# Kernel optimization log

Hardware: AMD Instinct MI355X
Metric: run time of the kernel (lower is better)

The kernel has to match this reference:

```python
import jax, jax.numpy as jnp
import numpy as np

GAMMA = 1.05  # VoxelSampler.GAMMA


def setup_inputs() -> dict:
    key = jax.random.key(0)
    k1, k2, k3, k4, k5 = jax.random.split(key, 5)
    B, T, R, Np, F = 2, 8, 128, 32768, 5
    # point xy within pc_range, remaining features (z, intensity, ...) gaussian
    xy = jax.random.uniform(k1, (B, T, Np, 2), minval=-75.0, maxval=75.0)
    rest = jax.random.normal(k2, (B, T, Np, F - 2))
    points = jnp.concatenate([xy, rest], axis=-1)  # [B,T,Np,5]
    # rois: [cx,cy,cz, dx,dy,dz, yaw, vx,vy]
    ctr = jax.random.uniform(k3, (B, T, R, 3), minval=-75.0, maxval=75.0)
    dims = jax.random.uniform(k4, (B, T, R, 3), minval=1.0, maxval=6.0)
    yaw_vel = jax.random.normal(k5, (B, T, R, 3))
    trajectory_rois = jnp.concatenate([ctr, dims, yaw_vel], axis=-1)  # [B,T,R,9]
    return {"points": points, "trajectory_rois": trajectory_rois, "num_sample": 32}


def reference(points, trajectory_rois, num_sample):
    # points: [B,T,Np,5] (pre-partitioned per batch/frame, mirrors the
    # batch-column + timestamp masking of the torch code with static shapes)
    # trajectory_rois: [B,T,R,9]
    B, T, R, _ = trajectory_rois.shape
    Fdim = points.shape[-1]
    # speed = ||roi[..., -2:]||, per-roi gamma = clamp((1.05*(1+speed))**(t/5), max=2.5)
    speed = jnp.linalg.norm(trajectory_rois[..., 7:9], axis=-1)          # [B,T,R]
    t_idx = jnp.arange(T, dtype=points.dtype)
    gamma = jnp.minimum((GAMMA * (1.0 + speed)) ** (t_idx[None, :, None] / 5.0), 2.5)
    # cylindrical radius per roi: ||dims_xy/2|| * gamma
    radiis = jnp.linalg.norm(trajectory_rois[..., 3:5] * 0.5, axis=-1) * gamma  # [B,T,R]
    cx = trajectory_rois[..., 0]
    cy = trajectory_rois[..., 1]
    px = points[..., 0]
    py = points[..., 1]
    dx = px[:, :, None, :] - cx[..., None]   # [B,T,R,Np]
    dy = py[:, :, None, :] - cy[..., None]
    dis = jnp.sqrt(dx * dx + dy * dy)        # [B,T,R,Np]
    in_radius = (dis <= radiis[..., None]).astype(points.dtype)
    # topk over 0/1 mask: picks num_sample in-radius points (lowest indices first),
    # exactly like torch.topk(point_mask.float(), num_sample)
    vals, idx = jax.lax.top_k(in_radius, num_sample)  # [B,T,R,S]
    sampled = jnp.take_along_axis(points[:, :, None, :, :], idx[..., None], axis=3)  # [B,T,R,S,5]
    sampled = jnp.where(vals[..., None] > 0, sampled, jnp.zeros((), dtype=points.dtype))
    # stack frames -> permute(0,2,1,3,4) -> flatten(2,3): [B,R,T*S,5]
    out = jnp.transpose(sampled, (0, 2, 1, 3, 4)).reshape(B, R, T * num_sample, Fdim)
    return out
```

## Files before the change

kernel.cpp:

```cpp
#include <hip/hip_runtime.h>
#include <math.h>

#define B_   2
#define T_   8
#define R_   128
#define NP_  32768
#define F_   5
#define S_   32
#define NBT  (B_ * T_)
#define NROW (NBT * R_)
#define WV_  8
#define SEGPTS (NP_ / WV_)
#define NIT  (SEGPTS / 512)

__device__ __forceinline__ int mbcnt64(unsigned long long m) {
    return __builtin_amdgcn_mbcnt_hi((unsigned)(m >> 32),
           __builtin_amdgcn_mbcnt_lo((unsigned)m, 0u));
}

__global__ __launch_bounds__(256) void xy_transpose_prep(
    const float* __restrict__ points,
    const float* __restrict__ rois,
    float2* __restrict__ xy,
    float4* __restrict__ rowc)
{
    const int j = blockIdx.x * blockDim.x + threadIdx.x;
    if (j < NBT * NP_ / 4) {
        const float4* src = (const float4*)points + (size_t)j * 5;
        const float4 a = src[0], b = src[1], c = src[2], d = src[3], e = src[4];
        float4* dst = (float4*)xy + (size_t)j * 2;
        dst[0] = make_float4(a.x, a.y, b.y, b.z);
        dst[1] = make_float4(c.z, c.w, d.w, e.x);
    }
    if (j < NROW) {
        const int row = j;
        const int bt  = row / R_;
        const int t   = bt % T_;
        const float* roi = rois + (size_t)row * 9;
        const float cx = roi[0], cy = roi[1];
        const float hx = roi[3] * 0.5f, hy = roi[4] * 0.5f;
        const float vx = roi[7], vy = roi[8];
        const float speed  = sqrtf(vx * vx + vy * vy);
        const float base_g = 1.05f * (1.0f + speed);
        const float expo   = (float)t / 5.0f;
        const float gamma  = fminf((float)pow((double)base_g, (double)expo), 2.5f);
        const float radius = sqrtf(hx * hx + hy * hy) * gamma;
        unsigned ut = __float_as_uint(radius * radius);
        while (sqrtf(__uint_as_float(ut)) > radius) --ut;
        while (sqrtf(__uint_as_float(ut + 1u)) <= radius) ++ut;
        rowc[row] = make_float4(cx, cy, __uint_as_float(ut), 0.0f);
    }
}


#define PROC(qq, kk)                                                              \
    {                                                                             \
        const int idx0 = segbase + (it * 256 + (kk) * 64 + lane) * 2;             \
        {     \
            const float ax = __fsub_rn(qq.x, rc0.x), ay = __fsub_rn(qq.y, rc0.y); \
            const float bx = __fsub_rn(qq.z, rc0.x), by = __fsub_rn(qq.w, rc0.y); \
            const float d2a = __fadd_rn(__fmul_rn(ax, ax), __fmul_rn(ay, ay));    \
            const float d2b = __fadd_rn(__fmul_rn(bx, bx), __fmul_rn(by, by));    \
            const bool p0 = (d2a <= rc0.z), p1 = (d2b <= rc0.z);                  \
            const unsigned long long m0 = __ballot(p0), m1 = __ballot(p1);        \
            if (m0 | m1) {                                                        \
                const int base = sel0 + mbcnt64(m0) + mbcnt64(m1);                \
                if (p0 && base < S_) hitbuf[w][0][base] = (unsigned short)idx0;   \
                if (p1) { const int s2 = base + (p0 ? 1 : 0);                     \
                          if (s2 < S_) hitbuf[w][0][s2] = (unsigned short)(idx0 + 1); } \
                sel0 += __popcll(m0) + __popcll(m1);                              \
            }                                                                     \
        }                                                                         \
        {                             \
            const float ax = __fsub_rn(qq.x, rc1.x), ay = __fsub_rn(qq.y, rc1.y); \
            const float bx = __fsub_rn(qq.z, rc1.x), by = __fsub_rn(qq.w, rc1.y); \
            const float d2a = __fadd_rn(__fmul_rn(ax, ax), __fmul_rn(ay, ay));    \
            const float d2b = __fadd_rn(__fmul_rn(bx, bx), __fmul_rn(by, by));    \
            const bool p0 = (d2a <= rc1.z), p1 = (d2b <= rc1.z);                  \
            const unsigned long long m0 = __ballot(p0), m1 = __ballot(p1);        \
            if (m0 | m1) {                                                        \
                const int base = sel1 + mbcnt64(m0) + mbcnt64(m1);                \
                if (p0 && base < S_) hitbuf[w][1][base] = (unsigned short)idx0;   \
                if (p1) { const int s2 = base + (p0 ? 1 : 0);                     \
                          if (s2 < S_) hitbuf[w][1][s2] = (unsigned short)(idx0 + 1); } \
                sel1 += __popcll(m0) + __popcll(m1);                              \
            }                                                                     \
        }                                                                         \
    }

__global__ __launch_bounds__(512) void fused_scan_emit(
    const float2* __restrict__ xy,
    const float4* __restrict__ rowc,
    const float* __restrict__ points,
    float* __restrict__ out)
{
    __shared__ unsigned short hitbuf[WV_][2][S_];
    __shared__ int cnt[WV_][2];
    const int w    = threadIdx.x >> 6;
    const int lane = threadIdx.x & 63;
    const int row0 = blockIdx.x * 2;
    const int row1 = row0 + 1;
    const int bt   = row0 / R_;
    const float4 rc0 = rowc[row0], rc1 = rowc[row1];
    const int segbase = w * SEGPTS;

    const float4* src = (const float4*)(xy + (size_t)bt * NP_) + (segbase >> 1) + lane;
    int sel0 = 0, sel1 = 0;
    float4 q0 = src[0], q1 = src[64], q2 = src[128], q3 = src[192];
    src += 256;
    int it = 0;
    for (; it < NIT - 1; ++it) {
        const float4 t0 = src[0], t1 = src[64], t2 = src[128], t3 = src[192];
        src += 256;
        PROC(q0, 0) PROC(q1, 1) PROC(q2, 2) PROC(q3, 3)
        q0 = t0; q1 = t1; q2 = t2; q3 = t3;
        if (sel0 >= S_ && sel1 >= S_) break;
    }
    if (it == NIT - 1) { PROC(q0, 0) PROC(q1, 1) PROC(q2, 2) PROC(q3, 3) }

    if (lane == 0) {
        cnt[w][0] = (sel0 < S_) ? sel0 : S_;
        cnt[w][1] = (sel1 < S_) ? sel1 : S_;
    }
    __syncthreads();

    if (threadIdx.x < 64) {
        const int half = lane >> 5;
        const int s    = lane & 31;
        int seg = -1, local = 0, acc = 0;
        #pragma unroll
        for (int g = 0; g < WV_; ++g) {
            const int na = acc + cnt[g][half];
            if (seg < 0 && s < na) { seg = g; local = s - acc; }
            acc = na;
        }
        const int row = half ? row1 : row0;
        const int r = row % R_;
        const int t = bt % T_;
        const int b = bt / T_;
        float* o = out + ((((size_t)b * R_ + r) * T_ + t) * S_ + s) * (size_t)F_;
        if (seg >= 0) {
            const int pi = hitbuf[seg][half][local];
            const float* p = points + ((size_t)bt * NP_ + pi) * F_;
            o[0] = p[0]; o[1] = p[1]; o[2] = p[2]; o[3] = p[3]; o[4] = p[4];
        } else {
            o[0] = 0.0f; o[1] = 0.0f; o[2] = 0.0f; o[3] = 0.0f; o[4] = 0.0f;
        }
    }
}

extern "C" void kernel_launch(void* const* d_in, const int* in_sizes, int n_in,
                              void* d_out, int out_size, void* d_ws, size_t ws_size,
                              hipStream_t stream) {
    const float* points = (const float*)d_in[0];
    const float* rois   = (const float*)d_in[1];
    float* out = (float*)d_out;

    char* ws = (char*)d_ws;
    float2* xy   = (float2*)ws;
    float4* rowc = (float4*)(ws + 4194304);

    xy_transpose_prep<<<(NBT * NP_ / 4 + 255) / 256, 256, 0, stream>>>(points, rois, xy, rowc);

    fused_scan_emit<<<NROW / 2, 512, 0, stream>>>(xy, rowc, points, out);
}
```

Before: 82.53 us.

## Process four ROI rows per block sharing each loaded point tile

Each block now tests four ROI rows against every loaded chunk of point xy data instead of two, halving the number of blocks and the global/L2 reads of the xy buffer per row. The main loop is restructured as a manually double-buffered pair of loads with no unrolling, and the early-exit check once all rows have 32 hits is removed, so every wave always scans its full segment. Launch bounds request higher occupancy. The trade-off is more registers and ballots per iteration, and losing the early termination when rows fill quickly.

New measurement: 84.81 us. +2.8%, slower.

```diff
diff --git a/kernel.cpp b/kernel.cpp
--- a/kernel.cpp
+++ b/kernel.cpp
@@ -10,6 +10,8 @@
 #define NBT  (B_ * T_)
 #define NROW (NBT * R_)
 #define WV_  8
+#define RPB  4
+#define NBLK (NROW / RPB)
 #define SEGPTS (NP_ / WV_)
 #define NIT  (SEGPTS / 512)
 
@@ -53,94 +55,99 @@
 }
 
 
-#define PROC(qq, kk)                                                              \
+#define PROC1(qq, base, rc, sel, hb)                                              \
     {                                                                             \
-        const int idx0 = segbase + (it * 256 + (kk) * 64 + lane) * 2;             \
-        {     \
-            const float ax = __fsub_rn(qq.x, rc0.x), ay = __fsub_rn(qq.y, rc0.y); \
-            const float bx = __fsub_rn(qq.z, rc0.x), by = __fsub_rn(qq.w, rc0.y); \
-            const float d2a = __fadd_rn(__fmul_rn(ax, ax), __fmul_rn(ay, ay));    \
-            const float d2b = __fadd_rn(__fmul_rn(bx, bx), __fmul_rn(by, by));    \
-            const bool p0 = (d2a <= rc0.z), p1 = (d2b <= rc0.z);                  \
-            const unsigned long long m0 = __ballot(p0), m1 = __ballot(p1);        \
-            if (m0 | m1) {                                                        \
-                const int base = sel0 + mbcnt64(m0) + mbcnt64(m1);                \
-                if (p0 && base < S_) hitbuf[w][0][base] = (unsigned short)idx0;   \
-                if (p1) { const int s2 = base + (p0 ? 1 : 0);                     \
-                          if (s2 < S_) hitbuf[w][0][s2] = (unsigned short)(idx0 + 1); } \
-                sel0 += __popcll(m0) + __popcll(m1);                              \
-            }                                                                     \
-        }                                                                         \
-        {                             \
-            const float ax = __fsub_rn(qq.x, rc1.x), ay = __fsub_rn(qq.y, rc1.y); \
-            const float bx = __fsub_rn(qq.z, rc1.x), by = __fsub_rn(qq.w, rc1.y); \
-            const float d2a = __fadd_rn(__fmul_rn(ax, ax), __fmul_rn(ay, ay));    \
-            const float d2b = __fadd_rn(__fmul_rn(bx, bx), __fmul_rn(by, by));    \
-            const bool p0 = (d2a <= rc1.z), p1 = (d2b <= rc1.z);                  \
-            const unsigned long long m0 = __ballot(p0), m1 = __ballot(p1);        \
-            if (m0 | m1) {                                                        \
-                const int base = sel1 + mbcnt64(m0) + mbcnt64(m1);                \
-                if (p0 && base < S_) hitbuf[w][1][base] = (unsigned short)idx0;   \
-                if (p1) { const int s2 = base + (p0 ? 1 : 0);                     \
-                          if (s2 < S_) hitbuf[w][1][s2] = (unsigned short)(idx0 + 1); } \
-                sel1 += __popcll(m0) + __popcll(m1);                              \
-            }                                                                     \
+        const float ax = __fsub_rn(qq.x, rc.x), ay = __fsub_rn(qq.y, rc.y);       \
+        const float bx = __fsub_rn(qq.z, rc.x), by = __fsub_rn(qq.w, rc.y);       \
+        const float d2a = __fadd_rn(__fmul_rn(ax, ax), __fmul_rn(ay, ay));        \
+        const float d2b = __fadd_rn(__fmul_rn(bx, bx), __fmul_rn(by, by));        \
+        const bool p0 = (d2a <= rc.z), p1 = (d2b <= rc.z);                        \
+        const unsigned long long m0 = __ballot(p0), m1 = __ballot(p1);            \
+        if (m0 | m1) {                                                            \
+            const int bb = sel + mbcnt64(m0) + mbcnt64(m1);                       \
+            if (p0 && bb < S_) hb[bb] = (unsigned short)((base) + l2);            \
+            if (p1) { const int s2 = bb + (p0 ? 1 : 0);                           \
+                      if (s2 < S_) hb[s2] = (unsigned short)((base) + l2 + 1); }  \
+            sel += __popcll(m0) + __popcll(m1);                                   \
         }                                                                         \
     }
 
-__global__ __launch_bounds__(512) void fused_scan_emit(
+#define PROCQ(qq, kk, ib)                                                         \
+    PROC1(qq, (ib) + (kk) * 128, rc0, sel0, hb0)                                  \
+    PROC1(qq, (ib) + (kk) * 128, rc1, sel1, hb1)                                  \
+    PROC1(qq, (ib) + (kk) * 128, rc2, sel2, hb2)                                  \
+    PROC1(qq, (ib) + (kk) * 128, rc3, sel3, hb3)
+
+#define LOAD4(r0, r1, r2, r3)                                                     \
+    r0 = src[0]; r1 = src[64]; r2 = src[128]; r3 = src[192]; src += 256;
+
+#define ITER(r0, r1, r2, r3, ib)                                                  \
+    PROCQ(r0, 0, ib) PROCQ(r1, 1, ib) PROCQ(r2, 2, ib) PROCQ(r3, 3, ib)
+
+__global__ __launch_bounds__(512, 4) void fused_scan_emit(
     const float2* __restrict__ xy,
     const float4* __restrict__ rowc,
     const float* __restrict__ points,
     float* __restrict__ out)
 {
-    __shared__ unsigned short hitbuf[WV_][2][S_];
-    __shared__ int cnt[WV_][2];
+    __shared__ unsigned short hitbuf[WV_][RPB][S_];
+    __shared__ int cnt[WV_][RPB];
     const int w    = threadIdx.x >> 6;
     const int lane = threadIdx.x & 63;
-    const int row0 = blockIdx.x * 2;
-    const int row1 = row0 + 1;
+    const int l2   = lane * 2;
+    const int row0 = blockIdx.x * RPB;
     const int bt   = row0 / R_;
-    const float4 rc0 = rowc[row0], rc1 = rowc[row1];
+    const float4 rc0 = rowc[row0], rc1 = rowc[row0 + 1];
+    const float4 rc2 = rowc[row0 + 2], rc3 = rowc[row0 + 3];
+    unsigned short* hb0 = hitbuf[w][0];
+    unsigned short* hb1 = hitbuf[w][1];
+    unsigned short* hb2 = hitbuf[w][2];
+    unsigned short* hb3 = hitbuf[w][3];
     const int segbase = w * SEGPTS;
 
     const float4* src = (const float4*)(xy + (size_t)bt * NP_) + (segbase >> 1) + lane;
-    int sel0 = 0, sel1 = 0;
-    float4 q0 = src[0], q1 = src[64], q2 = src[128], q3 = src[192];
-    src += 256;
-    int it = 0;
-    for (; it < NIT - 1; ++it) {
-        const float4 t0 = src[0], t1 = src[64], t2 = src[128], t3 = src[192];
-        src += 256;
-        PROC(q0, 0) PROC(q1, 1) PROC(q2, 2) PROC(q3, 3)
-        q0 = t0; q1 = t1; q2 = t2; q3 = t3;
-        if (sel0 >= S_ && sel1 >= S_) break;
+    int sel0 = 0, sel1 = 0, sel2 = 0, sel3 = 0;
+
+    float4 a0, a1, a2, a3, b0, b1, b2, b3;
+    LOAD4(a0, a1, a2, a3)
+    int ib = segbase;
+    #pragma unroll 1
+    for (int it = 0; it < NIT - 2; it += 2) {
+        LOAD4(b0, b1, b2, b3)
+        ITER(a0, a1, a2, a3, ib)
+        LOAD4(a0, a1, a2, a3)
+        ITER(b0, b1, b2, b3, ib + 512)
+        ib += 1024;
     }
-    if (it == NIT - 1) { PROC(q0, 0) PROC(q1, 1) PROC(q2, 2) PROC(q3, 3) }
+    LOAD4(b0, b1, b2, b3)
+    ITER(a0, a1, a2, a3, ib)
+    ITER(b0, b1, b2, b3, ib + 512)
 
     if (lane == 0) {
         cnt[w][0] = (sel0 < S_) ? sel0 : S_;
         cnt[w][1] = (sel1 < S_) ? sel1 : S_;
+        cnt[w][2] = (sel2 < S_) ? sel2 : S_;
+        cnt[w][3] = (sel3 < S_) ? sel3 : S_;
     }
     __syncthreads();
 
-    if (threadIdx.x < 64) {
-        const int half = lane >> 5;
-        const int s    = lane & 31;
+    if (threadIdx.x < RPB * S_) {
+        const int ri = threadIdx.x >> 5;
+        const int s  = threadIdx.x & 31;
         int seg = -1, local = 0, acc = 0;
         #pragma unroll
         for (int g = 0; g < WV_; ++g) {
-            const int na = acc + cnt[g][half];
+            const int na = acc + cnt[g][ri];
             if (seg < 0 && s < na) { seg = g; local = s - acc; }
             acc = na;
         }
-        const int row = half ? row1 : row0;
+        const int row = row0 + ri;
         const int r = row % R_;
         const int t = bt % T_;
         const int b = bt / T_;
         float* o = out + ((((size_t)b * R_ + r) * T_ + t) * S_ + s) * (size_t)F_;
         if (seg >= 0) {
-            const int pi = hitbuf[seg][half][local];
+            const int pi = hitbuf[seg][ri][local];
             const float* p = points + ((size_t)bt * NP_ + pi) * F_;
             o[0] = p[0]; o[1] = p[1]; o[2] = p[2]; o[3] = p[3]; o[4] = p[4];
         } else {
@@ -162,5 +169,5 @@
 
     xy_transpose_prep<<<(NBT * NP_ / 4 + 255) / 256, 256, 0, stream>>>(points, rois, xy, rowc);
 
-    fused_scan_emit<<<NROW / 2, 512, 0, stream>>>(xy, rowc, points, out);
+    fused_scan_emit<<<NBLK, 512, 0, stream>>>(xy, rowc, points, out);
 }
```
